# Kernel tuning notes

Measured on AMD Instinct MI355X. Metric: run time of the kernel, lower is better.

The kernel has to match this reference:

```python
import jax, jax.numpy as jnp
import numpy as np

D_MODEL = 256
MLP_DIM = 1024
EPS = 1e-5

def _layernorm(x, g, b):
    mu = jnp.mean(x, axis=-1, keepdims=True)
    var = jnp.mean(jnp.square(x - mu), axis=-1, keepdims=True)
    return (x - mu) * jax.lax.rsqrt(var + EPS) * g + b

def setup_inputs() -> dict:
    key = jax.random.key(0)
    ks = jax.random.split(key, 4)
    d, m = D_MODEL, MLP_DIM
    x = jax.random.normal(ks[0], (8, 1024, 4, d), dtype=jnp.float32)
    w_qkv = jax.random.normal(ks[1], (3 * d, d), dtype=jnp.float32) * 0.05  # torch Linear weight (out,in)
    gamma1 = jnp.ones((d,), jnp.float32)
    beta1 = jnp.zeros((d,), jnp.float32)
    gamma2 = jnp.ones((d,), jnp.float32)
    beta2 = jnp.zeros((d,), jnp.float32)
    w1 = jax.random.normal(ks[2], (m, d), dtype=jnp.float32) * 0.05
    b1 = jnp.zeros((m,), jnp.float32)
    w2 = jax.random.normal(ks[3], (d, m), dtype=jnp.float32) * 0.05
    b2 = jnp.zeros((d,), jnp.float32)
    return {"x": x, "w_qkv": w_qkv, "gamma1": gamma1, "beta1": beta1,
            "gamma2": gamma2, "beta2": beta2, "w1": w1, "b1": b1, "w2": w2, "b2": b2}

def reference(x, w_qkv, gamma1, beta1, gamma2, beta2, w1, b1, w2, b2):
    bsz, n, h, d = x.shape
    scale = d ** -0.5
    # --- attention branch: x + attn(norm1(x)) ---
    xn = _layernorm(x, gamma1, beta1)
    # Linear(d, 3d): xn @ W^T, then reshape trailing 3d -> (d, 3) as in torch
    qkv = jnp.einsum('bnhd,ed->bnhe', xn, w_qkv).reshape(bsz, n * h, d, 3)
    q, k, v = qkv[..., 0], qkv[..., 1], qkv[..., 2]   # [b, n*h, d]
    dots = jnp.einsum('bid,bjd->bij', q, k) * scale   # [b, n*h, n*h]
    attn = jax.nn.softmax(dots, axis=-1)              # dropout=0 -> identity
    out = jnp.einsum('bij,bjd->bid', attn, v).reshape(bsz, n, h, d)
    x = x + out
    # --- mlp branch: x + mlp(norm2(x)) ---
    xn2 = _layernorm(x, gamma2, beta2)
    hid = jax.nn.silu(jnp.einsum('bnhd,md->bnhm', xn2, w1) + b1)
    x = x + jnp.einsum('bnhm,dm->bnhd', hid, w2) + b2
    return x
```

## Files before the change

kernel.cpp:

```cpp
#include <hip/hip_runtime.h>


typedef __attribute__((ext_vector_type(8))) short bf16x8;
typedef __attribute__((ext_vector_type(4))) short bf16x4;
typedef __attribute__((ext_vector_type(4))) float f32x4;
typedef __attribute__((ext_vector_type(16))) float f32x16;

static __device__ __forceinline__ short f2bf(float f) {
    union { float f; unsigned u; } v; v.f = f;
    unsigned r = (v.u + 0x7FFFu + ((v.u >> 16) & 1u)) >> 16;
    return (short)r;
}

static __device__ __forceinline__ void gll16(const void* g, void* l) {
    __builtin_amdgcn_global_load_lds(
        (const __attribute__((address_space(1))) unsigned*)g,
        (__attribute__((address_space(3))) unsigned*)l, 16, 0, 0);
}

__global__ __launch_bounds__(256) void k_cvt(const float* __restrict__ wqkv,
                                             const float* __restrict__ w1,
                                             const float* __restrict__ w2,
                                             short* __restrict__ owqkv,
                                             short* __restrict__ ow1,
                                             short* __restrict__ ow2) {
    int i = blockIdx.x * 256 + threadIdx.x;
    if (i < 196608) {
        int e = i >> 8, col = i & 255;
        int dd = e / 3, which = e - dd * 3;
        float v = wqkv[i];
        if (which == 0) v *= 0.0625f * 1.44269504f;
        owqkv[((which << 8) + dd) * 256 + col] = f2bf(v);
    }
    if (i < 262144) { ow1[i] = f2bf(w1[i]); ow2[i] = f2bf(w2[i]); }
}

__global__ __launch_bounds__(256) void k_ln(const float* __restrict__ x,
                                            const float* __restrict__ g,
                                            const float* __restrict__ bta,
                                            short* __restrict__ out) {
    int w = threadIdx.x >> 6, lane = threadIdx.x & 63;
    long row = (long)blockIdx.x * 4 + w;
    float4 v = *((const float4*)(x + row * 256) + lane);
    float s = v.x + v.y + v.z + v.w;
    float q = v.x * v.x + v.y * v.y + v.z * v.z + v.w * v.w;
    for (int off = 1; off < 64; off <<= 1) {
        s += __shfl_xor(s, off);
        q += __shfl_xor(q, off);
    }
    float mean = s * (1.0f / 256.0f);
    float var = q * (1.0f / 256.0f) - mean * mean;
    float rstd = rsqrtf(var + 1e-5f);
    float4 gg = *((const float4*)g + lane);
    float4 bb = *((const float4*)bta + lane);
    short4 o;
    o.x = f2bf((v.x - mean) * rstd * gg.x + bb.x);
    o.y = f2bf((v.y - mean) * rstd * gg.y + bb.y);
    o.z = f2bf((v.z - mean) * rstd * gg.z + bb.z);
    o.w = f2bf((v.w - mean) * rstd * gg.w + bb.w);
    *((short4*)(out + row * 256) + lane) = o;
}

__global__ __launch_bounds__(256) void k_qkv(const short* __restrict__ xn,
                                             const short* __restrict__ wb,
                                             short* __restrict__ Q,
                                             short* __restrict__ K,
                                             short* __restrict__ VT) {
    __shared__ __attribute__((aligned(16))) short lds_a[64 * 264];
    __shared__ __attribute__((aligned(16))) short lds_b[64 * 264];
    int t = threadIdx.x;
    int m0 = blockIdx.y * 64, n0 = blockIdx.x * 64;
    const int4* ga = (const int4*)xn;
    const int4* gb = (const int4*)wb;
    int4* la = (int4*)lds_a;
    int4* lb = (int4*)lds_b;
    for (int it = 0; it < 8; it++) {
        int c = t + 256 * it;
        int r = c >> 5, k = c & 31;
        la[r * 33 + k] = ga[(long)(m0 + r) * 32 + k];
        lb[r * 33 + k] = gb[(n0 + r) * 32 + k];
    }
    __syncthreads();
    int w = t >> 6, lane = t & 63, ln = lane & 15, qd = lane >> 4;
    int moff = (w >> 1) * 32, noff = (w & 1) * 32;
    f32x4 acc[2][2] = {};
    for (int ks = 0; ks < 8; ks++) {
        bf16x8 a0 = *(const bf16x8*)&lds_a[(moff + ln) * 264 + ks * 32 + qd * 8];
        bf16x8 a1 = *(const bf16x8*)&lds_a[(moff + 16 + ln) * 264 + ks * 32 + qd * 8];
        bf16x8 b0 = *(const bf16x8*)&lds_b[(noff + ln) * 264 + ks * 32 + qd * 8];
        bf16x8 b1 = *(const bf16x8*)&lds_b[(noff + 16 + ln) * 264 + ks * 32 + qd * 8];
        acc[0][0] = __builtin_amdgcn_mfma_f32_16x16x32_bf16(a0, b0, acc[0][0], 0, 0, 0);
        acc[0][1] = __builtin_amdgcn_mfma_f32_16x16x32_bf16(a0, b1, acc[0][1], 0, 0, 0);
        acc[1][0] = __builtin_amdgcn_mfma_f32_16x16x32_bf16(a1, b0, acc[1][0], 0, 0, 0);
        acc[1][1] = __builtin_amdgcn_mfma_f32_16x16x32_bf16(a1, b1, acc[1][1], 0, 0, 0);
    }
    for (int mi = 0; mi < 2; mi++)
        for (int nj = 0; nj < 2; nj++)
            for (int rg = 0; rg < 4; rg++) {
                float v = acc[mi][nj][rg];
                int gr = m0 + moff + mi * 16 + qd * 4 + rg;
                int e = n0 + noff + nj * 16 + ln;
                int which = e >> 8, dd = e & 255;
                short bv = f2bf(v);
                if (which == 0) Q[(long)gr * 256 + dd] = bv;
                else if (which == 1) K[(long)gr * 256 + dd] = bv;
                else {
                    int b = gr >> 12, i = gr & 4095;
                    VT[((long)b * 256 + dd) * 4096 + i] = bv;
                }
            }
}

__global__ __launch_bounds__(256, 1) void k_attn(const short* __restrict__ Q,
                                                 const short* __restrict__ K,
                                                 const short* __restrict__ VT,
                                                 const float* __restrict__ x,
                                                 float* __restrict__ out) {
    __shared__ __attribute__((aligned(16))) short lds_k[2][32 * 256];
    __shared__ __attribute__((aligned(16))) short lds_v[2][256 * 32];
    int t = threadIdx.x, w = t >> 6, l = t & 63, l5 = l & 31, h = l >> 5;
    int b = blockIdx.y;
    int q0 = blockIdx.x * 128 + w * 32;

    bf16x8 qf[16];
    {
        const short* qrow = Q + ((long)(b * 4096 + q0 + l5)) * 256;
        #pragma unroll
        for (int kc = 0; kc < 16; kc++) qf[kc] = *(const bf16x8*)(qrow + kc * 16 + h * 8);
    }
    f32x16 O[8] = {};
    float lsum = 0.f;

    const char* Kb = (const char*)(K + (long)b * 4096 * 256);
    const int4* gv = (const int4*)(VT + (long)b * 4096 * 256);

    long koff[4]; int klds[4];
    #pragma unroll
    for (int i = 0; i < 4; i++) {
        int r = w * 8 + i * 2 + (l >> 5);
        koff[i] = (long)r * 512 + (long)((l5 ^ (r & 31)) * 16);
        klds[i] = (w * 8 + i * 2) * 512;
    }
    int4 vs[4];

    #pragma unroll
    for (int i = 0; i < 4; i++) {
        int c = t + 256 * i;
        vs[i] = gv[(c >> 2) * 512 + (c & 3)];
    }
    #pragma unroll
    for (int i = 0; i < 4; i++) gll16(Kb + koff[i], (char*)lds_k[0] + klds[i]);
    #pragma unroll
    for (int i = 0; i < 4; i++) {
        int c = t + 256 * i, d = c >> 2, ch = c & 3;
        char* base = (char*)lds_v[0] + d * 64;
        *(int2*)(base + (((ch * 2 + 0) ^ (d & 7)) * 8)) = make_int2(vs[i].x, vs[i].y);
        *(int2*)(base + (((ch * 2 + 1) ^ (d & 7)) * 8)) = make_int2(vs[i].z, vs[i].w);
    }
    __syncthreads();

    for (int jt = 0; jt < 128; jt++) {
        int cur = jt & 1;
        if (jt < 127) {
            #pragma unroll
            for (int i = 0; i < 4; i++) {
                int c = t + 256 * i;
                vs[i] = gv[(c >> 2) * 512 + (jt + 1) * 4 + (c & 3)];
            }
            long ka = (long)(jt + 1) * 16384;
            #pragma unroll
            for (int i = 0; i < 4; i++)
                gll16(Kb + ka + koff[i], (char*)lds_k[cur ^ 1] + klds[i]);
        }
        const short* lk = lds_k[cur];
        const short* lv = lds_v[cur];
        f32x16 st = {};
        #pragma unroll
        for (int kc = 0; kc < 16; kc++) {
            int cc = kc * 2 + h;
            bf16x8 a = *(const bf16x8*)(lk + (l5 * 32 + (cc ^ l5)) * 8);
            st = __builtin_amdgcn_mfma_f32_32x32x16_bf16(a, qf[kc], st, 0, 0, 0);
        }
        bf16x4 pf[4];
        #pragma unroll
        for (int r4 = 0; r4 < 4; r4++) {
            float p0 = __builtin_amdgcn_exp2f(st[r4 * 4 + 0]);
            float p1 = __builtin_amdgcn_exp2f(st[r4 * 4 + 1]);
            float p2 = __builtin_amdgcn_exp2f(st[r4 * 4 + 2]);
            float p3 = __builtin_amdgcn_exp2f(st[r4 * 4 + 3]);
            lsum += (p0 + p1) + (p2 + p3);
            union { float f; unsigned u; } u0, u1, u2, u3;
            u0.f = p0; u1.f = p1; u2.f = p2; u3.f = p3;
            union { unsigned u[2]; bf16x4 v; } pk;
            pk.u[0] = __builtin_amdgcn_perm(u1.u + 0x8000u, u0.u + 0x8000u, 0x07060302u);
            pk.u[1] = __builtin_amdgcn_perm(u3.u + 0x8000u, u2.u + 0x8000u, 0x07060302u);
            pf[r4] = pk.v;
        }
        #pragma unroll
        for (int dt = 0; dt < 8; dt++) {
            int d = dt * 32 + l5;
            const char* vbase = (const char*)lv + d * 64;
            #pragma unroll
            for (int k4 = 0; k4 < 4; k4++) {
                bf16x4 va = *(const bf16x4*)(vbase + (((k4 * 2 + h) ^ (d & 7)) * 8));
                O[dt] = __builtin_amdgcn_mfma_f32_32x32x8bf16_1k(va, pf[k4], O[dt], 0, 0, 0);
            }
        }
        if (jt < 127) {
            #pragma unroll
            for (int i = 0; i < 4; i++) {
                int c = t + 256 * i, d = c >> 2, ch = c & 3;
                char* base = (char*)lds_v[cur ^ 1] + d * 64;
                *(int2*)(base + (((ch * 2 + 0) ^ (d & 7)) * 8)) = make_int2(vs[i].x, vs[i].y);
                *(int2*)(base + (((ch * 2 + 1) ^ (d & 7)) * 8)) = make_int2(vs[i].z, vs[i].w);
            }
        }
        __syncthreads();
    }

    float lt = lsum + __shfl_xor(lsum, 32);
    float rinv = 1.0f / lt;
    float* fscr = (float*)lds_k[0] + w * (32 * 33);
    #pragma unroll
    for (int dt = 0; dt < 8; dt++) {
        #pragma unroll
        for (int r = 0; r < 16; r++) {
            int drow = (r & 3) + 8 * (r >> 2) + 4 * h;
            fscr[drow * 33 + l5] = O[dt][r] * rinv;
        }
        asm volatile("s_waitcnt lgkmcnt(0)" ::: "memory");
        #pragma unroll
        for (int it = 0; it < 16; it++) {
            int ql = it * 2 + h;
            float v = fscr[l5 * 33 + ql];
            long idx = ((long)(b * 4096 + q0 + ql)) * 256 + dt * 32 + l5;
            out[idx] = x[idx] + v;
        }
        asm volatile("s_waitcnt lgkmcnt(0)" ::: "memory");
    }
}

__global__ __launch_bounds__(256) void k_mlp(const short* __restrict__ xn,
                                             const short* __restrict__ w1b,
                                             const short* __restrict__ w2b,
                                             const float* __restrict__ b1,
                                             const float* __restrict__ b2,
                                             float* __restrict__ out) {
    __shared__ __attribute__((aligned(16))) short lds_w[2][16 * 256];
    __shared__ __attribute__((aligned(16))) short lds_h[4][16 * 264];
    int t = threadIdx.x, w = t >> 6, l = t & 63, ln = l & 15, qd = l >> 4;
    int R0 = blockIdx.x * 64 + w * 16;
    short* lhs = lds_h[w];

    bf16x8 a1f[8];
    #pragma unroll
    for (int kc = 0; kc < 8; kc++)
        a1f[kc] = *(const bf16x8*)(xn + (long)(R0 + ln) * 256 + kc * 32 + qd * 8);

    int rr[2]; long s1off[2], s2off[2]; int wlds[2];
    #pragma unroll
    for (int i = 0; i < 2; i++) {
        int r = w * 4 + i * 2 + (l >> 5);
        int ch = (l & 31) ^ r;
        rr[i] = r;
        s1off[i] = (long)r * 512 + ch * 16;
        s2off[i] = (long)r * 2048 + ch * 16;
        wlds[i] = (w * 4 + i * 2) * 512;
    }
    const char* W1c = (const char*)w1b;
    const char* W2c = (const char*)w2b;

    f32x4 Oc[16] = {};
    #pragma unroll
    for (int i = 0; i < 2; i++)
        gll16(W1c + s1off[i], (char*)lds_w[0] + wlds[i]);
    __syncthreads();
    int cur = 0;

    for (int pass = 0; pass < 4; pass++) {
        for (int nt = 0; nt < 16; nt++) {
            if (nt < 15) {
                long base = (long)(pass * 256 + (nt + 1) * 16) * 512;
                #pragma unroll
                for (int i = 0; i < 2; i++)
                    gll16(W1c + base + s1off[i], (char*)lds_w[cur ^ 1] + wlds[i]);
            } else {
                long base = (long)pass * 512;
                #pragma unroll
                for (int i = 0; i < 2; i++)
                    gll16(W2c + base + s2off[i], (char*)lds_w[cur ^ 1] + wlds[i]);
            }
            f32x4 acc = {};
            const short* lw = lds_w[cur];
            #pragma unroll
            for (int kc = 0; kc < 8; kc++) {
                int cc = kc * 4 + qd;
                bf16x8 bf = *(const bf16x8*)(lw + (ln * 32 + (cc ^ ln)) * 8);
                acc = __builtin_amdgcn_mfma_f32_16x16x32_bf16(a1f[kc], bf, acc, 0, 0, 0);
            }
            float bb = b1[pass * 256 + nt * 16 + ln];
            #pragma unroll
            for (int rg = 0; rg < 4; rg++) {
                float z = acc[rg] + bb;
                float sv = z / (1.0f + __expf(-z));
                lhs[(qd * 4 + rg) * 264 + nt * 16 + ln] = f2bf(sv);
            }
            __syncthreads();
            cur ^= 1;
        }
        bf16x8 a2f[8];
        #pragma unroll
        for (int kc = 0; kc < 8; kc++)
            a2f[kc] = *(const bf16x8*)&lhs[ln * 264 + kc * 32 + qd * 8];
        for (int nt = 0; nt < 16; nt++) {
            if (nt < 15) {
                long base = (long)((nt + 1) * 16) * 2048 + (long)pass * 512;
                #pragma unroll
                for (int i = 0; i < 2; i++)
                    gll16(W2c + base + s2off[i], (char*)lds_w[cur ^ 1] + wlds[i]);
            } else if (pass < 3) {
                long base = (long)((pass + 1) * 256) * 512;
                #pragma unroll
                for (int i = 0; i < 2; i++)
                    gll16(W1c + base + s1off[i], (char*)lds_w[cur ^ 1] + wlds[i]);
            }
            const short* lw = lds_w[cur];
            #pragma unroll
            for (int kc = 0; kc < 8; kc++) {
                int cc = kc * 4 + qd;
                bf16x8 bf = *(const bf16x8*)(lw + (ln * 32 + (cc ^ ln)) * 8);
                Oc[nt] = __builtin_amdgcn_mfma_f32_16x16x32_bf16(a2f[kc], bf, Oc[nt], 0, 0, 0);
            }
            __syncthreads();
            cur ^= 1;
        }
    }
    for (int nt = 0; nt < 16; nt++) {
        int dd = nt * 16 + ln;
        float bb = b2[dd];
        #pragma unroll
        for (int rg = 0; rg < 4; rg++) {
            long idx = (long)(R0 + qd * 4 + rg) * 256 + dd;
            out[idx] = out[idx] + Oc[nt][rg] + bb;
        }
    }
}

extern "C" void kernel_launch(void* const* d_in, const int* in_sizes, int n_in,
                              void* d_out, int out_size, void* d_ws, size_t ws_size,
                              hipStream_t stream) {
    const float* x    = (const float*)d_in[0];
    const float* wqkv = (const float*)d_in[1];
    const float* g1   = (const float*)d_in[2];
    const float* be1  = (const float*)d_in[3];
    const float* g2   = (const float*)d_in[4];
    const float* be2  = (const float*)d_in[5];
    const float* w1   = (const float*)d_in[6];
    const float* b1   = (const float*)d_in[7];
    const float* w2   = (const float*)d_in[8];
    const float* b2   = (const float*)d_in[9];
    float* out = (float*)d_out;
    char* ws = (char*)d_ws;
    short* WQKV = (short*)(ws);
    short* W1B  = (short*)(ws + (512l << 10));
    short* W2B  = (short*)(ws + (1l << 20));
    short* XN   = (short*)(ws + (2l << 20));
    short* Qb   = (short*)(ws + (18l << 20));
    short* Kb   = (short*)(ws + (34l << 20));
    short* VTb  = (short*)(ws + (50l << 20));

    k_cvt<<<1024, 256, 0, stream>>>(wqkv, w1, w2, WQKV, W1B, W2B);
    k_ln<<<8192, 256, 0, stream>>>(x, g1, be1, XN);
    k_qkv<<<dim3(12, 512), 256, 0, stream>>>(XN, WQKV, Qb, Kb, VTb);
    k_attn<<<dim3(32, 8), 256, 0, stream>>>(Qb, Kb, VTb, x, out);
    k_ln<<<8192, 256, 0, stream>>>(out, g2, be2, XN);
    k_mlp<<<512, 256, 0, stream>>>(XN, W1B, W2B, b1, b2, out);
}
```

Measured before the change: 475.9 us.

## Use 32x32x16 bf16 MFMA for PV with permlane32 swap and padded V LDS

Switches the P·V product in the attention kernel from the 32x32x8 MFMA (bf16x4 operands) to the 32x32x16 MFMA (bf16x8 operands), halving the number of MFMA issues and LDS reads for V. The P fragments are rearranged across wave halves with v_permlane32_swap to match the K=16 operand layout. The V tile in LDS switches from an XOR swizzle with 8-byte stores to a row padding of 80 bytes with 16-byte stores and loads. This increases the LDS footprint and relies on the lane permutation matching the MFMA operand layout exactly.

```diff
diff --git a/kernel.cpp b/kernel.cpp
--- a/kernel.cpp
+++ b/kernel.cpp
@@ -117,7 +117,7 @@
                                                  const float* __restrict__ x,
                                                  float* __restrict__ out) {
     __shared__ __attribute__((aligned(16))) short lds_k[2][32 * 256];
-    __shared__ __attribute__((aligned(16))) short lds_v[2][256 * 32];
+    __shared__ __attribute__((aligned(16))) short lds_v[2][256 * 40];
     int t = threadIdx.x, w = t >> 6, l = t & 63, l5 = l & 31, h = l >> 5;
     int b = blockIdx.y;
     int q0 = blockIdx.x * 128 + w * 32;
@@ -153,9 +153,7 @@
     #pragma unroll
     for (int i = 0; i < 4; i++) {
         int c = t + 256 * i, d = c >> 2, ch = c & 3;
-        char* base = (char*)lds_v[0] + d * 64;
-        *(int2*)(base + (((ch * 2 + 0) ^ (d & 7)) * 8)) = make_int2(vs[i].x, vs[i].y);
-        *(int2*)(base + (((ch * 2 + 1) ^ (d & 7)) * 8)) = make_int2(vs[i].z, vs[i].w);
+        *(int4*)((char*)lds_v[0] + d * 80 + ch * 16) = vs[i];
     }
     __syncthreads();
 
@@ -181,7 +179,7 @@
             bf16x8 a = *(const bf16x8*)(lk + (l5 * 32 + (cc ^ l5)) * 8);
             st = __builtin_amdgcn_mfma_f32_32x32x16_bf16(a, qf[kc], st, 0, 0, 0);
         }
-        bf16x4 pf[4];
+        unsigned pw[4][2];
         #pragma unroll
         for (int r4 = 0; r4 < 4; r4++) {
             float p0 = __builtin_amdgcn_exp2f(st[r4 * 4 + 0]);
@@ -191,28 +189,34 @@
             lsum += (p0 + p1) + (p2 + p3);
             union { float f; unsigned u; } u0, u1, u2, u3;
             u0.f = p0; u1.f = p1; u2.f = p2; u3.f = p3;
-            union { unsigned u[2]; bf16x4 v; } pk;
-            pk.u[0] = __builtin_amdgcn_perm(u1.u + 0x8000u, u0.u + 0x8000u, 0x07060302u);
-            pk.u[1] = __builtin_amdgcn_perm(u3.u + 0x8000u, u2.u + 0x8000u, 0x07060302u);
-            pf[r4] = pk.v;
+            pw[r4][0] = __builtin_amdgcn_perm(u1.u + 0x8000u, u0.u + 0x8000u, 0x07060302u);
+            pw[r4][1] = __builtin_amdgcn_perm(u3.u + 0x8000u, u2.u + 0x8000u, 0x07060302u);
+        }
+        bf16x8 pfr[2];
+        #pragma unroll
+        for (int k2 = 0; k2 < 2; k2++) {
+            unsigned a0 = pw[2 * k2][0], a1 = pw[2 * k2][1];
+            unsigned b0 = pw[2 * k2 + 1][0], b1 = pw[2 * k2 + 1][1];
+            asm("v_permlane32_swap_b32 %0, %1" : "+v"(a0), "+v"(b0));
+            asm("v_permlane32_swap_b32 %0, %1" : "+v"(a1), "+v"(b1));
+            union { unsigned u[4]; bf16x8 v; } f;
+            f.u[0] = a0; f.u[1] = a1; f.u[2] = b0; f.u[3] = b1;
+            pfr[k2] = f.v;
         }
         #pragma unroll
         for (int dt = 0; dt < 8; dt++) {
-            int d = dt * 32 + l5;
-            const char* vbase = (const char*)lv + d * 64;
-            #pragma unroll
-            for (int k4 = 0; k4 < 4; k4++) {
-                bf16x4 va = *(const bf16x4*)(vbase + (((k4 * 2 + h) ^ (d & 7)) * 8));
-                O[dt] = __builtin_amdgcn_mfma_f32_32x32x8bf16_1k(va, pf[k4], O[dt], 0, 0, 0);
+            const char* vbase = (const char*)lv + (dt * 32 + l5) * 80;
+            #pragma unroll
+            for (int k2 = 0; k2 < 2; k2++) {
+                bf16x8 va = *(const bf16x8*)(vbase + (k2 * 2 + h) * 16);
+                O[dt] = __builtin_amdgcn_mfma_f32_32x32x16_bf16(va, pfr[k2], O[dt], 0, 0, 0);
             }
         }
         if (jt < 127) {
             #pragma unroll
             for (int i = 0; i < 4; i++) {
                 int c = t + 256 * i, d = c >> 2, ch = c & 3;
-                char* base = (char*)lds_v[cur ^ 1] + d * 64;
-                *(int2*)(base + (((ch * 2 + 0) ^ (d & 7)) * 8)) = make_int2(vs[i].x, vs[i].y);
-                *(int2*)(base + (((ch * 2 + 1) ^ (d & 7)) * 8)) = make_int2(vs[i].z, vs[i].w);
+                *(int4*)((char*)lds_v[cur ^ 1] + d * 80 + ch * 16) = vs[i];
             }
         }
         __syncthreads();
```

After: 566.5 us. +19.0%, slower.
